# Optimization experiments

Hardware: AMD Instinct MI355X
Metric: run time of the kernel (lower is better)

Reference implementation:

```python
import jax, jax.numpy as jnp
import numpy as np

KERNEL_SIZE = 32
KERNEL_STRIDE = 16
HEAD_NUM_K = 4
HEAD_DIM = 128
BATCH = 4
SEQ_LEN = 16384


def _calc_chunks_with_stride(cu_seqlens_np, chunk_size, stride):
    """Mirror of calc_chunks_with_stride using numpy (index computation on host).

    Returns flat gather indices (num_chunks*chunk_size,) and compressed
    cumulative sequence lengths (batch+1,).
    """
    cu = np.asarray(cu_seqlens_np, dtype=np.int64)
    batch_sizes = cu[1:] - cu[:-1]
    max_seq_len = int(batch_sizes.max())
    max_chunks = max((max_seq_len - chunk_size) // stride + 1, 0)
    offsets = np.arange(0, max_chunks * stride, stride, dtype=np.int64)  # (C,)
    seq_starts = cu[:-1]
    chunk_start = seq_starts[:, None] + offsets[None, :]            # (B, C)
    chunk_end = chunk_start + chunk_size
    valid = chunk_end <= (seq_starts[:, None] + batch_sizes[:, None])  # (B, C)
    valid_starts = chunk_start[valid]                               # (N,)
    inner = np.arange(chunk_size, dtype=np.int64)[None, :]          # (1, K)
    flat_idx = (valid_starts[:, None] + inner).reshape(-1)          # (N*K,)
    n_per_batch = valid.sum(axis=1)
    cu_comp = np.zeros(len(cu), dtype=np.int32)
    cu_comp[1:] = np.cumsum(n_per_batch)
    return flat_idx, cu_comp


def setup_inputs() -> dict:
    key = jax.random.key(0)
    k = jax.random.normal(key, (BATCH * SEQ_LEN, HEAD_NUM_K, HEAD_DIM), dtype=jnp.float32)
    cu_seqlens = jnp.arange(BATCH + 1, dtype=jnp.int32) * SEQ_LEN
    return {"k": k, "cu_seqlens": cu_seqlens}


def reference(k, cu_seqlens):
    # Index computation is data-dependent on concrete cu_seqlens (host-side).
    flat_idx, cu_comp = _calc_chunks_with_stride(np.asarray(cu_seqlens), KERNEL_SIZE, KERNEL_STRIDE)
    idx = jnp.asarray(flat_idx)
    # Gather overlapping chunks: (N*K, H, D) -> (N, K, H, D) -> mean over K.
    gathered = k[idx]
    gathered = gathered.reshape(-1, KERNEL_SIZE, HEAD_NUM_K, HEAD_DIM)
    compressed_k = gathered.mean(axis=1)
    return compressed_k, jnp.asarray(cu_comp)
```

## Files before the change

### kernel.cpp

```cpp
#include <hip/hip_runtime.h>

#define KSIZE   32
#define KSTRIDE 16
#define HK      4
#define HD      128
#define ROW     (HK * HD)
#define BATCH   4
#define SEQLEN  16384
#define CHUNKS_PER_BATCH ((SEQLEN - KSIZE) / KSTRIDE + 1)
#define TOTAL_CHUNKS     (BATCH * CHUNKS_PER_BATCH)

__global__ __launch_bounds__(128)
void compress_k_kernel(const float* __restrict__ k,
                       const int* __restrict__ cu_seqlens,
                       float* __restrict__ out) {
    const int chunk = blockIdx.x;
    const int b = chunk / CHUNKS_PER_BATCH;
    const int c = chunk - b * CHUNKS_PER_BATCH;
    const long start_row = (long)cu_seqlens[b] + (long)c * KSTRIDE;

    const float4* __restrict__ src =
        (const float4*)(k + start_row * ROW);
    const int t = threadIdx.x;

    float4 acc = make_float4(0.f, 0.f, 0.f, 0.f);
    #pragma unroll
    for (int i = 0; i < KSIZE; ++i) {
        float4 v = src[(long)i * (ROW / 4) + t];
        acc.x += v.x; acc.y += v.y; acc.z += v.z; acc.w += v.w;
    }
    const float s = 1.0f / (float)KSIZE;
    float4 r = make_float4(acc.x * s, acc.y * s, acc.z * s, acc.w * s);
    ((float4*)(out + (long)chunk * ROW))[t] = r;
}

__global__ void cu_comp_kernel(const int* __restrict__ cu_seqlens,
                               float* __restrict__ tail) {
    if (threadIdx.x == 0 && blockIdx.x == 0) {
        int run = 0;
        tail[0] = 0.0f;
        #pragma unroll
        for (int b = 0; b < BATCH; ++b) {
            const int len = cu_seqlens[b + 1] - cu_seqlens[b];
            const int n = (len >= KSIZE) ? (len - KSIZE) / KSTRIDE + 1 : 0;
            run += n;
            tail[b + 1] = (float)run;
        }
    }
}

extern "C" void kernel_launch(void* const* d_in, const int* in_sizes, int n_in,
                              void* d_out, int out_size, void* d_ws, size_t ws_size,
                              hipStream_t stream) {
    const float* k          = (const float*)d_in[0];
    const int*   cu_seqlens = (const int*)d_in[1];
    float*       out        = (float*)d_out;

    float* tail = out + (long)TOTAL_CHUNKS * ROW;

    compress_k_kernel<<<TOTAL_CHUNKS, 128, 0, stream>>>(k, cu_seqlens, out);
    cu_comp_kernel<<<1, 64, 0, stream>>>(cu_seqlens, tail);
}
```

Before: 197.4 us.

## Share half-window partial sums across three adjacent chunks per block and fuse kernels

Each block now handles three consecutive chunks. Because stride is half the window, it sums four 16-row halves once and combines neighbouring halves for each output, instead of re-reading the full 32 rows per chunk. This cuts redundant global/cache reads from 2x the input to about 4/3x. The separate single-thread cu_comp kernel is folded into block 0, removing a launch. The cost is more registers per thread and fewer blocks in the grid.

```diff
diff --git a/kernel.cpp b/kernel.cpp
--- a/kernel.cpp
+++ b/kernel.cpp
@@ -5,46 +5,63 @@
 #define HK      4
 #define HD      128
 #define ROW     (HK * HD)
+#define ROW4    (ROW / 4)
 #define BATCH   4
 #define SEQLEN  16384
 #define CHUNKS_PER_BATCH ((SEQLEN - KSIZE) / KSTRIDE + 1)
 #define TOTAL_CHUNKS     (BATCH * CHUNKS_PER_BATCH)
 
+#define G 3
+#define BLOCKS_PER_BATCH (CHUNKS_PER_BATCH / G)
+#define TOTAL_BLOCKS     (BATCH * BLOCKS_PER_BATCH)
+
 __global__ __launch_bounds__(128)
-void compress_k_kernel(const float* __restrict__ k,
-                       const int* __restrict__ cu_seqlens,
-                       float* __restrict__ out) {
-    const int chunk = blockIdx.x;
-    const int b = chunk / CHUNKS_PER_BATCH;
-    const int c = chunk - b * CHUNKS_PER_BATCH;
-    const long start_row = (long)cu_seqlens[b] + (long)c * KSTRIDE;
+void compress_k_fused(const float* __restrict__ k,
+                      const int* __restrict__ cu_seqlens,
+                      float* __restrict__ out,
+                      float* __restrict__ tail) {
+    const int blk = blockIdx.x;
+    const int b   = blk / BLOCKS_PER_BATCH;
+    const int cb  = blk - b * BLOCKS_PER_BATCH;
+    const int c0  = cb * G;
 
-    const float4* __restrict__ src =
-        (const float4*)(k + start_row * ROW);
+    const long start_row = (long)cu_seqlens[b] + (long)c0 * KSTRIDE;
+    const float4* __restrict__ src = (const float4*)(k + start_row * ROW);
     const int t = threadIdx.x;
 
-    float4 acc = make_float4(0.f, 0.f, 0.f, 0.f);
+    float4 h[G + 1];
     #pragma unroll
-    for (int i = 0; i < KSIZE; ++i) {
-        float4 v = src[(long)i * (ROW / 4) + t];
-        acc.x += v.x; acc.y += v.y; acc.z += v.z; acc.w += v.w;
+    for (int j = 0; j <= G; ++j) h[j] = make_float4(0.f, 0.f, 0.f, 0.f);
+
+    #pragma unroll
+    for (int j = 0; j <= G; ++j) {
+        #pragma unroll
+        for (int i = 0; i < KSTRIDE; ++i) {
+            float4 v = src[(long)(j * KSTRIDE + i) * ROW4 + t];
+            h[j].x += v.x; h[j].y += v.y; h[j].z += v.z; h[j].w += v.w;
+        }
     }
+
     const float s = 1.0f / (float)KSIZE;
-    float4 r = make_float4(acc.x * s, acc.y * s, acc.z * s, acc.w * s);
-    ((float4*)(out + (long)chunk * ROW))[t] = r;
-}
+    const int chunk0 = b * CHUNKS_PER_BATCH + c0;
+    #pragma unroll
+    for (int g = 0; g < G; ++g) {
+        float4 r = make_float4((h[g].x + h[g + 1].x) * s,
+                               (h[g].y + h[g + 1].y) * s,
+                               (h[g].z + h[g + 1].z) * s,
+                               (h[g].w + h[g + 1].w) * s);
+        ((float4*)(out + (long)(chunk0 + g) * ROW))[t] = r;
+    }
 
-__global__ void cu_comp_kernel(const int* __restrict__ cu_seqlens,
-                               float* __restrict__ tail) {
-    if (threadIdx.x == 0 && blockIdx.x == 0) {
+    if (blk == 0 && t == 0) {
         int run = 0;
         tail[0] = 0.0f;
         #pragma unroll
-        for (int b = 0; b < BATCH; ++b) {
-            const int len = cu_seqlens[b + 1] - cu_seqlens[b];
+        for (int i = 0; i < BATCH; ++i) {
+            const int len = cu_seqlens[i + 1] - cu_seqlens[i];
             const int n = (len >= KSIZE) ? (len - KSIZE) / KSTRIDE + 1 : 0;
             run += n;
-            tail[b + 1] = (float)run;
+            tail[i + 1] = (float)run;
         }
     }
 }
@@ -55,9 +72,7 @@
     const float* k          = (const float*)d_in[0];
     const int*   cu_seqlens = (const int*)d_in[1];
     float*       out        = (float*)d_out;
+    float*       tail       = out + (long)TOTAL_CHUNKS * ROW;
 
-    float* tail = out + (long)TOTAL_CHUNKS * ROW;
-
-    compress_k_kernel<<<TOTAL_CHUNKS, 128, 0, stream>>>(k, cu_seqlens, out);
-    cu_comp_kernel<<<1, 64, 0, stream>>>(cu_seqlens, tail);
+    compress_k_fused<<<TOTAL_BLOCKS, 128, 0, stream>>>(k, cu_seqlens, out, tail);
 }
```

New measurement: 195.7 us (median of 2 runs). No clear change (-0.9%).
